# Performance work log

Measured on AMD Instinct MI355X. Metric: run time of the kernel, lower is better.

The kernel has to match this reference:

```python
import jax, jax.numpy as jnp
import numpy as np

N, K, D = 100000, 512, 256
DECAY = 0.99


def _cdist(a, b):
    # Euclidean pairwise distance, like torch.cdist (p=2)
    d2 = (jnp.sum(a * a, axis=1)[:, None]
          + jnp.sum(b * b, axis=1)[None, :]
          - 2.0 * a @ b.T)
    return jnp.sqrt(jnp.maximum(d2, 0.0))


def setup_inputs() -> dict:
    key = jax.random.key(0)
    kx, = jax.random.split(key, 1)
    x = jax.random.normal(kx, (N, D), dtype=jnp.float32)
    # 'random' init picks rows of x; using the first K rows guarantees each
    # centroid is its own nearest point -> every cluster non-empty.
    centroids = x[:K]
    # prev_assignments equals the current argmin so the EMA update branch fires
    prev_assignments = jnp.argmin(_cdist(x, centroids), axis=1).astype(jnp.int64)
    return {"x": x, "centroids": centroids, "prev_assignments": prev_assignments}


def reference(x, centroids, prev_assignments):
    distances = _cdist(x, centroids)            # [N, K]
    new_assignments = jnp.argmin(distances, axis=1)  # [N]
    match = jnp.all(new_assignments == prev_assignments)

    def _do_update(_):
        # one-hot scatter accumulation == segment_sum over assignments
        sums = jax.ops.segment_sum(x, new_assignments, num_segments=K)   # [K, D]
        counts = jax.ops.segment_sum(jnp.ones((x.shape[0],), x.dtype),
                                     new_assignments, num_segments=K)    # [K]
        new_c = sums / counts[:, None]
        updated = (1.0 - DECAY) * centroids + DECAY * new_c
        # recompute assignments against updated centroids
        a2 = jnp.argmin(_cdist(x, updated), axis=1)
        return a2, updated, jnp.bool_(True)

    def _no_update(_):
        return new_assignments, centroids, jnp.bool_(False)

    assignments_out, centroids_out, updated_flag = jax.lax.cond(
        match, _do_update, _no_update, None)
    return assignments_out, updated_flag, centroids_out
```

## Files before the change

kernel.cpp:

```cpp
#include <hip/hip_runtime.h>
#include <math.h>

#define DD 256
#define KK 512
#define TM 64
#define TKC 128
#define NCHUNK 4
#define DSL 32
#define NSL 8
#define NSLICES 32
#define SPLIT 8

typedef float float4v __attribute__((ext_vector_type(4)));
typedef float float2v __attribute__((ext_vector_type(2)));

__device__ __forceinline__ void gld_lds16(const void* g, void* l) {
    __builtin_amdgcn_global_load_lds((const __attribute__((address_space(1))) void*)g,
                                     (__attribute__((address_space(3))) void*)l, 16, 0, 0);
}

template<bool FIRST>
__global__ __launch_bounds__(256, 2)
void argmin_kernel(const float* __restrict__ x, const float* __restrict__ cent,
                   const float* __restrict__ cc,
                   const int N,
                   int* __restrict__ assign_out,
                   const int* __restrict__ prev, const int pstride,
                   unsigned int* __restrict__ mismatch,
                   int* __restrict__ counts)
{
    __shared__ float xs[2][TM * DSL];
    __shared__ float cs[2][TKC * DSL];

    const int tid  = threadIdx.x;
    const int w    = tid >> 6;
    const int lane = tid & 63;
    const int tr   = tid >> 4;
    const int tc   = tid & 15;
    const long long rowbase = (long long)blockIdx.x * TM;

    float minv[4]; int mini[4];
#pragma unroll
    for (int i = 0; i < 4; ++i) { minv[i] = __builtin_inff(); mini[i] = 0; }

    const int r_st  = (w << 3) + (lane >> 3);
    const int slot4 = (lane & 7) << 2;

#define STAGE(BUF, S) do {                                                        \
        const int d0_    = ((S) & 7) * DSL;                                       \
        const int cbase_ = ((S) >> 3) * TKC;                                      \
        _Pragma("unroll")                                                         \
        for (int call = 0; call < 4; ++call) {                                    \
            int r  = (call << 5) + r_st;                                          \
            int dl = slot4 ^ (((r >> 2) & 7) << 2);                               \
            gld_lds16(cent + (long long)(cbase_ + r) * DD + d0_ + dl,             \
                      &cs[(BUF)][((call << 2) + w) << 8]);                        \
            if (call < 2) {                                                       \
                long long p = rowbase + r; if (p > N - 1) p = N - 1;              \
                gld_lds16(x + p * DD + d0_ + dl,                                  \
                          &xs[(BUF)][((call << 2) + w) << 8]);                    \
            }                                                                     \
        }                                                                         \
    } while (0)

    STAGE(0, 0);
    int s = 0;
    float2v acc2[4][8];

#pragma unroll 1
    for (int chunk = 0; chunk < NCHUNK; ++chunk) {
        float cchalf[8];
#pragma unroll
        for (int j = 0; j < 8; ++j) {
            int r = ((j >> 2) << 6) + (tc << 2) + (j & 3);
            cchalf[j] = 0.5f * cc[chunk * TKC + r];
        }
#pragma unroll
        for (int i = 0; i < 4; ++i)
#pragma unroll
            for (int j = 0; j < 8; ++j) acc2[i][j] = (float2v){0.0f, 0.0f};

#pragma unroll 1
        for (int sl = 0; sl < NSL; ++sl) {
            const int buf = s & 1;
            __syncthreads();
            if (s + 1 < NSLICES) STAGE(buf ^ 1, s + 1);
#pragma unroll
            for (int g = 0; g < 8; ++g) {
                const int dl = g << 2;
                float4v ax[4], bc[8];
#pragma unroll
                for (int i = 0; i < 4; ++i) {
                    int r = (tr << 2) + i;
                    ax[i] = *(const float4v*)&xs[buf][(r << 5) + (dl ^ (((r >> 2) & 7) << 2))];
                }
#pragma unroll
                for (int j = 0; j < 8; ++j) {
                    int r = ((j >> 2) << 6) + (tc << 2) + (j & 3);
                    bc[j] = *(const float4v*)&cs[buf][(r << 5) + (dl ^ (((r >> 2) & 7) << 2))];
                }
#pragma unroll
                for (int i = 0; i < 4; ++i) {
                    const float2v axl = __builtin_shufflevector(ax[i], ax[i], 0, 1);
                    const float2v axh = __builtin_shufflevector(ax[i], ax[i], 2, 3);
#pragma unroll
                    for (int j = 0; j < 8; ++j) {
                        const float2v bcl = __builtin_shufflevector(bc[j], bc[j], 0, 1);
                        const float2v bch = __builtin_shufflevector(bc[j], bc[j], 2, 3);
                        float2v t = acc2[i][j];
                        t = __builtin_elementwise_fma(axl, bcl, t);
                        t = __builtin_elementwise_fma(axh, bch, t);
                        acc2[i][j] = t;
                    }
                }
            }
            ++s;
        }
        {
#pragma clang fp contract(off)
#pragma unroll
            for (int i = 0; i < 4; ++i)
#pragma unroll
                for (int j = 0; j < 8; ++j) {
                    int r = ((j >> 2) << 6) + (tc << 2) + (j & 3);
                    float dot   = acc2[i][j][0] + acc2[i][j][1];
                    float score = cchalf[j] - dot;
                    if (score < minv[i]) { minv[i] = score; mini[i] = chunk * TKC + r; }
                }
        }
    }
#undef STAGE

#pragma unroll
    for (int i = 0; i < 4; ++i) {
#pragma unroll
        for (int off = 1; off < 16; off <<= 1) {
            float ov = __shfl_xor(minv[i], off);
            int   oi = __shfl_xor(mini[i], off);
            if (ov < minv[i] || (ov == minv[i] && oi < mini[i])) { minv[i] = ov; mini[i] = oi; }
        }
    }
    if (tc == 0) {
        unsigned int mis = 0;
#pragma unroll
        for (int i = 0; i < 4; ++i) {
            long long p = rowbase + (tr << 2) + i;
            if (p < N) {
                assign_out[p] = mini[i];
                if (FIRST) {
                    atomicAdd(&counts[mini[i]], 1);
                }
                if (prev != nullptr && prev[p * pstride] != mini[i]) ++mis;
            }
        }
        if (mis) atomicAdd(mismatch, mis);
    }
}

__global__ void sqnorm_kernel(const float* __restrict__ m, float* __restrict__ out, const int n)
{
    const int w = threadIdx.x >> 6, lane = threadIdx.x & 63;
    const int row = (blockIdx.x << 2) + w;
    if (row >= n) return;
    const float4v v = *(const float4v*)&m[(long long)row * DD + (lane << 2)];
    float s = v[0]*v[0] + v[1]*v[1] + v[2]*v[2] + v[3]*v[3];
#pragma unroll
    for (int off = 1; off < 64; off <<= 1) s += __shfl_xor(s, off);
    if (lane == 0) out[row] = s;
}

__global__ __launch_bounds__(KK)
void scan_kernel(const int* __restrict__ counts, int* __restrict__ starts, int* __restrict__ cursor)
{
    __shared__ int buf[2][KK];
    const int t = threadIdx.x;
    const int v = counts[t];
    buf[0][t] = v;
    __syncthreads();
    int src = 0;
#pragma unroll
    for (int off = 1; off < KK; off <<= 1) {
        int val = buf[src][t];
        if (t >= off) val += buf[src][t - off];
        buf[src ^ 1][t] = val;
        src ^= 1;
        __syncthreads();
    }
    const int excl = buf[src][t] - v;
    starts[t] = excl;
    cursor[t] = excl;
}

__global__ void scatter_kernel(const int* __restrict__ assign, int* __restrict__ cursor,
                               int* __restrict__ idx, const int N)
{
    const int p = blockIdx.x * 256 + threadIdx.x;
    if (p >= N) return;
    const int a = assign[p];
    const int pos = atomicAdd(&cursor[a], 1);
    idx[pos] = p;
}

__global__ __launch_bounds__(256)
void gather_kernel(const float* __restrict__ x, const int* __restrict__ idx,
                   const int* __restrict__ starts, const int* __restrict__ counts,
                   unsigned long long* __restrict__ sums)
{
    const int c    = blockIdx.x / SPLIT;
    const int part = blockIdx.x % SPLIT;
    const int d    = threadIdx.x;
    const int start = starts[c], cnt = counts[c];
    const int chunk = (cnt + SPLIT - 1) / SPLIT;
    const int i0 = part * chunk;
    int i1 = i0 + chunk; if (i1 > cnt) i1 = cnt;
    if (i1 <= i0) return;

    long long acc = 0;
    int i = i0;
    for (; i + 4 <= i1; i += 4) {
        const int p0 = idx[start + i + 0];
        const int p1 = idx[start + i + 1];
        const int p2 = idx[start + i + 2];
        const int p3 = idx[start + i + 3];
        const float v0 = x[(long long)p0 * DD + d];
        const float v1 = x[(long long)p1 * DD + d];
        const float v2 = x[(long long)p2 * DD + d];
        const float v3 = x[(long long)p3 * DD + d];
        acc += __double2ll_rn((double)v0 * 1099511627776.0);
        acc += __double2ll_rn((double)v1 * 1099511627776.0);
        acc += __double2ll_rn((double)v2 * 1099511627776.0);
        acc += __double2ll_rn((double)v3 * 1099511627776.0);
    }
    for (; i < i1; ++i) {
        const int p = idx[start + i];
        acc += __double2ll_rn((double)x[(long long)p * DD + d] * 1099511627776.0);
    }
    atomicAdd(&sums[(size_t)c * DD + d], (unsigned long long)acc);
}

__global__ void update_kernel(const float* __restrict__ cent,
                              const unsigned long long* __restrict__ sums,
                              const int* __restrict__ counts,
                              float* __restrict__ updated, float* __restrict__ cc2)
{
    const int c = blockIdx.x, d = threadIdx.x;
    const int w = d >> 6, lane = d & 63;
    __shared__ float red[4];
    float u;
    {
#pragma clang fp contract(off)
        const float cnt = (float)counts[c];
        const float sf  = (float)((double)(long long)sums[(size_t)c * DD + d] * (1.0 / 1099511627776.0));
        const float nc  = sf / cnt;
        u = 0.01f * cent[(size_t)c * DD + d] + 0.99f * nc;
    }
    updated[(size_t)c * DD + d] = u;
    float s = u * u;
#pragma unroll
    for (int off = 1; off < 64; off <<= 1) s += __shfl_xor(s, off);
    if (lane == 0) red[w] = s;
    __syncthreads();
    if (d == 0) cc2[c] = (red[0] + red[1]) + (red[2] + red[3]);
}

__global__ void output_kernel(const unsigned int* __restrict__ mismatch,
                              const int* __restrict__ a1, const int* __restrict__ a2,
                              const float* __restrict__ cent, const float* __restrict__ updated,
                              float* __restrict__ out, const int N, const int total)
{
    const int g = blockIdx.x * 256 + threadIdx.x;
    if (g >= total) return;
    const bool match = (*mismatch == 0u);
    if (g < N)       out[g] = (float)(match ? a2[g] : a1[g]);
    else if (g == N) out[g] = match ? 1.0f : 0.0f;
    else {
        const int e = g - N - 1;
        out[g] = match ? updated[e] : cent[e];
    }
}

extern "C" void kernel_launch(void* const* d_in, const int* in_sizes, int n_in,
                              void* d_out, int out_size, void* d_ws, size_t ws_size,
                              hipStream_t stream)
{
    const float* x    = (const float*)d_in[0];
    const float* cent = (const float*)d_in[1];
    const int*   prev = (const int*)d_in[2];
    const int N = in_sizes[0] / DD;
    const int pstride = (n_in >= 3 && in_sizes[2] >= 2 * N) ? 2 : 1;

    char* ws = (char*)d_ws;
    size_t off = 0;
    auto alloc = [&](size_t b) { void* p = ws + off; off += (b + 255) & ~(size_t)255; return p; };
    int*   assign1 = (int*)alloc((size_t)N * 4);
    int*   assign2 = (int*)alloc((size_t)N * 4);
    float* cc      = (float*)alloc(KK * 4);
    float* cc2v    = (float*)alloc(KK * 4);
    int*   counts  = (int*)alloc(KK * 4);
    int*   starts  = (int*)alloc(KK * 4);
    int*   cursor  = (int*)alloc(KK * 4);
    int*   idx     = (int*)alloc((size_t)N * 4);
    unsigned long long* sums = (unsigned long long*)alloc((size_t)KK * DD * 8);
    float* updated = (float*)alloc((size_t)KK * DD * 4);
    unsigned int* mismatch = (unsigned int*)alloc(256);

    hipMemsetAsync(counts, 0, KK * 4, stream);
    hipMemsetAsync(sums, 0, (size_t)KK * DD * 8, stream);
    hipMemsetAsync(mismatch, 0, 4, stream);

    sqnorm_kernel<<<(KK + 3) / 4, 256, 0, stream>>>(cent, cc, KK);

    const int gb = (N + TM - 1) / TM;
    argmin_kernel<true><<<gb, 256, 0, stream>>>(x, cent, cc, N, assign1,
                                                prev, pstride, mismatch, counts);

    scan_kernel<<<1, KK, 0, stream>>>(counts, starts, cursor);
    scatter_kernel<<<(N + 255) / 256, 256, 0, stream>>>(assign1, cursor, idx, N);
    gather_kernel<<<KK * SPLIT, 256, 0, stream>>>(x, idx, starts, counts, sums);

    update_kernel<<<KK, 256, 0, stream>>>(cent, sums, counts, updated, cc2v);

    argmin_kernel<false><<<gb, 256, 0, stream>>>(x, updated, cc2v, N, assign2,
                                                 nullptr, 1, nullptr, nullptr);

    output_kernel<<<(out_size + 255) / 256, 256, 0, stream>>>(mismatch, assign1, assign2,
                                                              cent, updated, (float*)d_out,
                                                              N, out_size);
}
```

Baseline: 1.042 ms.

## Double argmin row tile to 128 rows per block with two accumulator sets

Raises the row tile from 64 to 128 so each thread computes an 8x8 register tile (two 4x8 halves) against the same centroid fragments, doubling reuse of each centroid LDS load and halving total centroid global traffic. X staging now loads four rows per call instead of two. This doubles accumulator registers (64 float2 per thread), which under launch_bounds(256,2) risks spilling or lower occupancy, and halves the number of blocks in the grid.

```diff
diff --git a/kernel.cpp b/kernel.cpp
--- a/kernel.cpp
+++ b/kernel.cpp
@@ -3,7 +3,7 @@
 
 #define DD 256
 #define KK 512
-#define TM 64
+#define TM 128
 #define TKC 128
 #define NCHUNK 4
 #define DSL 32
@@ -39,9 +39,9 @@
     const int tc   = tid & 15;
     const long long rowbase = (long long)blockIdx.x * TM;
 
-    float minv[4]; int mini[4];
-#pragma unroll
-    for (int i = 0; i < 4; ++i) { minv[i] = __builtin_inff(); mini[i] = 0; }
+    float minv[8]; int mini[8];
+#pragma unroll
+    for (int i = 0; i < 8; ++i) { minv[i] = __builtin_inff(); mini[i] = 0; }
 
     const int r_st  = (w << 3) + (lane >> 3);
     const int slot4 = (lane & 7) << 2;
@@ -53,19 +53,17 @@
         for (int call = 0; call < 4; ++call) {                                    \
             int r  = (call << 5) + r_st;                                          \
             int dl = slot4 ^ (((r >> 2) & 7) << 2);                               \
+            long long p = rowbase + r; if (p > N - 1) p = N - 1;                  \
+            gld_lds16(x + p * DD + d0_ + dl, &xs[(BUF)][((call << 2) + w) << 8]); \
             gld_lds16(cent + (long long)(cbase_ + r) * DD + d0_ + dl,             \
                       &cs[(BUF)][((call << 2) + w) << 8]);                        \
-            if (call < 2) {                                                       \
-                long long p = rowbase + r; if (p > N - 1) p = N - 1;              \
-                gld_lds16(x + p * DD + d0_ + dl,                                  \
-                          &xs[(BUF)][((call << 2) + w) << 8]);                    \
-            }                                                                     \
         }                                                                         \
     } while (0)
 
     STAGE(0, 0);
     int s = 0;
-    float2v acc2[4][8];
+    float2v accA[4][8];
+    float2v accB[4][8];
 
 #pragma unroll 1
     for (int chunk = 0; chunk < NCHUNK; ++chunk) {
@@ -78,7 +76,10 @@
 #pragma unroll
         for (int i = 0; i < 4; ++i)
 #pragma unroll
-            for (int j = 0; j < 8; ++j) acc2[i][j] = (float2v){0.0f, 0.0f};
+            for (int j = 0; j < 8; ++j) {
+                accA[i][j] = (float2v){0.0f, 0.0f};
+                accB[i][j] = (float2v){0.0f, 0.0f};
+            }
 
 #pragma unroll 1
         for (int sl = 0; sl < NSL; ++sl) {
@@ -88,12 +89,7 @@
 #pragma unroll
             for (int g = 0; g < 8; ++g) {
                 const int dl = g << 2;
-                float4v ax[4], bc[8];
-#pragma unroll
-                for (int i = 0; i < 4; ++i) {
-                    int r = (tr << 2) + i;
-                    ax[i] = *(const float4v*)&xs[buf][(r << 5) + (dl ^ (((r >> 2) & 7) << 2))];
-                }
+                float4v bc[8];
 #pragma unroll
                 for (int j = 0; j < 8; ++j) {
                     int r = ((j >> 2) << 6) + (tc << 2) + (j & 3);
@@ -101,16 +97,36 @@
                 }
 #pragma unroll
                 for (int i = 0; i < 4; ++i) {
-                    const float2v axl = __builtin_shufflevector(ax[i], ax[i], 0, 1);
-                    const float2v axh = __builtin_shufflevector(ax[i], ax[i], 2, 3);
+                    int r = (tr << 2) + i;
+                    const float4v ax =
+                        *(const float4v*)&xs[buf][(r << 5) + (dl ^ (((r >> 2) & 7) << 2))];
+                    const float2v axl = __builtin_shufflevector(ax, ax, 0, 1);
+                    const float2v axh = __builtin_shufflevector(ax, ax, 2, 3);
 #pragma unroll
                     for (int j = 0; j < 8; ++j) {
                         const float2v bcl = __builtin_shufflevector(bc[j], bc[j], 0, 1);
                         const float2v bch = __builtin_shufflevector(bc[j], bc[j], 2, 3);
-                        float2v t = acc2[i][j];
+                        float2v t = accA[i][j];
                         t = __builtin_elementwise_fma(axl, bcl, t);
                         t = __builtin_elementwise_fma(axh, bch, t);
-                        acc2[i][j] = t;
+                        accA[i][j] = t;
+                    }
+                }
+#pragma unroll
+                for (int i = 0; i < 4; ++i) {
+                    int r = 64 + (tr << 2) + i;
+                    const float4v ax =
+                        *(const float4v*)&xs[buf][(r << 5) + (dl ^ (((r >> 2) & 7) << 2))];
+                    const float2v axl = __builtin_shufflevector(ax, ax, 0, 1);
+                    const float2v axh = __builtin_shufflevector(ax, ax, 2, 3);
+#pragma unroll
+                    for (int j = 0; j < 8; ++j) {
+                        const float2v bcl = __builtin_shufflevector(bc[j], bc[j], 0, 1);
+                        const float2v bch = __builtin_shufflevector(bc[j], bc[j], 2, 3);
+                        float2v t = accB[i][j];
+                        t = __builtin_elementwise_fma(axl, bcl, t);
+                        t = __builtin_elementwise_fma(axh, bch, t);
+                        accB[i][j] = t;
                     }
                 }
             }
@@ -123,16 +139,20 @@
 #pragma unroll
                 for (int j = 0; j < 8; ++j) {
                     int r = ((j >> 2) << 6) + (tc << 2) + (j & 3);
-                    float dot   = acc2[i][j][0] + acc2[i][j][1];
-                    float score = cchalf[j] - dot;
-                    if (score < minv[i]) { minv[i] = score; mini[i] = chunk * TKC + r; }
+                    const int cidx = chunk * TKC + r;
+                    float dotA   = accA[i][j][0] + accA[i][j][1];
+                    float scoreA = cchalf[j] - dotA;
+                    if (scoreA < minv[i])     { minv[i]     = scoreA; mini[i]     = cidx; }
+                    float dotB   = accB[i][j][0] + accB[i][j][1];
+                    float scoreB = cchalf[j] - dotB;
+                    if (scoreB < minv[4 + i]) { minv[4 + i] = scoreB; mini[4 + i] = cidx; }
                 }
         }
     }
 #undef STAGE
 
 #pragma unroll
-    for (int i = 0; i < 4; ++i) {
+    for (int i = 0; i < 8; ++i) {
 #pragma unroll
         for (int off = 1; off < 16; off <<= 1) {
             float ov = __shfl_xor(minv[i], off);
@@ -143,8 +163,8 @@
     if (tc == 0) {
         unsigned int mis = 0;
 #pragma unroll
-        for (int i = 0; i < 4; ++i) {
-            long long p = rowbase + (tr << 2) + i;
+        for (int i = 0; i < 8; ++i) {
+            long long p = rowbase + ((i >> 2) << 6) + (tr << 2) + (i & 3);
             if (p < N) {
                 assign_out[p] = mini[i];
                 if (FIRST) {
```

After: 1.055 ms. Within noise of the previous version (+1.2%).
